# Kernel tuning notes

Measured on AMD Instinct MI355X. Metric: run time of the kernel, lower is better.

The kernel has to match this reference:

```python
import math
import jax, jax.numpy as jnp
from jax import lax
import numpy as np

SR = 48000
N_SAMPLES = 1_440_000
N_TRACKS = 4  # voice, music, ambient, fx

# ---------------- EQ (peaking biquads, Direct Form II transposed) ----------------

def _peak_coefs(freq, gain_db, q):
    A = 10.0 ** (gain_db / 40.0)
    w0 = 2.0 * math.pi * freq / SR
    al = math.sin(w0) / (2.0 * q)
    a0 = 1.0 + al / A
    return ((1.0 + al * A) / a0, -2.0 * math.cos(w0) / a0, (1.0 - al * A) / a0,
            -2.0 * math.cos(w0) / a0, (1.0 - al / A) / a0)

_IDENT = (1.0, 0.0, 0.0, 0.0, 0.0)  # pass-through biquad for padding
_PRESETS = {
    'voice':   [(300.0, -3.0, 0.7), (3000.0, 3.0, 1.0), (8000.0, 2.0, 0.7)],
    'music':   [(80.0, 2.0, 0.7), (5000.0, 1.0, 1.0)],
    'ambient': [(200.0, -2.0, 0.7), (6000.0, -1.0, 0.7)],
    'fx':      [(1000.0, 2.0, 1.0)],
}
_TYPES = ('voice', 'music', 'ambient', 'fx')

def _stage_coefs():
    # [3 stages, 4 tracks, 5 coefs]; missing bands padded with identity biquads
    out = np.zeros((3, N_TRACKS, 5), np.float32)
    for t, ty in enumerate(_TYPES):
        bands = [_peak_coefs(*b) for b in _PRESETS[ty]]
        bands += [_IDENT] * (3 - len(bands))
        for s in range(3):
            out[s, t] = bands[s]
    return out

STAGE_COEFS = _stage_coefs()

def _biquad(x, c):
    # x: [T, C, N], c: [T, 5] -> batched DF2T biquad across tracks/channels
    b0, b1, b2, a1, a2 = (c[:, i][:, None] for i in range(5))
    def step(carry, x_n):  # x_n: [T, C]
        z1, z2 = carry
        y = b0 * x_n + z1
        return (b1 * x_n - a1 * y + z2, b2 * x_n - a2 * y), y
    z = jnp.zeros_like(x[..., 0])
    _, ys = lax.scan(step, (z, z), jnp.moveaxis(x, -1, 0))
    return jnp.moveaxis(ys, 0, -1)

# ---------------- Compressor (envelope follower) ----------------
ATK = math.exp(-1.0 / (10.0 * 0.001 * SR))
REL = math.exp(-1.0 / (100.0 * 0.001 * SR))
THR = 10.0 ** (-18.0 / 20.0)
GR_EXP = 1.0 / 4.0 - 1.0  # ratio = 4

def _compress(x):
    def step(env, x_n):
        lvl = jnp.abs(x_n)
        c = jnp.where(lvl > env, ATK, REL)
        env = c * env + (1.0 - c) * lvl
        gr = jnp.maximum(env / (THR + 1e-8), 1.0) ** GR_EXP
        return env, x_n * gr
    _, ys = lax.scan(step, jnp.zeros_like(x[..., 0]), jnp.moveaxis(x, -1, 0))
    return jnp.moveaxis(ys, 0, -1)

# ---------------- Reverb (Schroeder-Moorer: 4 comb + 2 allpass) ----------------
_BASE = int(SR * 0.03)
COMB_DELAYS = [_BASE, int(_BASE * 1.13), int(_BASE * 1.27), int(_BASE * 1.41)]
AP_DELAYS = [int(SR * 0.005), int(SR * 0.0017)]
FB = 0.3 + 0.5 * 0.6  # room_size = 0.6
WET = 0.3

def _comb(x, delay, fb):
    # y[n] = x[n] + fb*y[n-delay]: `delay` independent 1st-order recurrences
    T, C, N = x.shape
    M = -(-N // delay)
    xp = jnp.pad(x, ((0, 0), (0, 0), (0, M * delay - N))).reshape(T, C, M, delay)
    def step(carry, xm):  # carry/xm: [T, C, delay]
        y = xm + fb * carry
        return y, y
    _, ys = lax.scan(step, jnp.zeros_like(xp[:, :, 0]), jnp.moveaxis(xp, 2, 0))
    return jnp.moveaxis(ys, 0, 2).reshape(T, C, M * delay)[:, :, :N]

def _allpass(x, delay, fb):
    # y[n] = -fb*x[n] + x[n-delay] + fb*y[n-delay] for n>=delay, y[0:delay]=0
    T, C, N = x.shape
    M = -(-N // delay)
    xp = jnp.pad(x, ((0, 0), (0, 0), (0, M * delay - N))).reshape(T, C, M, delay)
    xs = jnp.moveaxis(xp, 2, 0)  # [M, T, C, delay]
    y0 = jnp.zeros_like(xs[0])
    def step(carry, xm):
        x_prev, y_prev = carry
        y = -fb * xm + x_prev + fb * y_prev
        return (xm, y), y
    _, ys = lax.scan(step, (xs[0], y0), xs[1:])
    ys = jnp.concatenate([y0[None], ys], axis=0)
    return jnp.moveaxis(ys, 0, 2).reshape(T, C, M * delay)[:, :, :N]

def _reverb(x):
    wet = sum(_comb(x, d, FB) for d in COMB_DELAYS) / float(len(COMB_DELAYS))
    for d in AP_DELAYS:
        wet = _allpass(wet, d, FB)
    return (1.0 - WET) * x + WET * wet

# ---------------- Full mixer ----------------
CEIL = 10.0 ** (-1.0 / 20.0)  # limiter ceiling, -1 dB

def _forward(tracks, volumes, pans):
    x = tracks  # [4, 2, N]
    for s in range(3):
        x = _biquad(x, jnp.asarray(STAGE_COEFS[s]))
    x = _compress(x)
    # reverb only for ambient (idx 2) and fx (idx 3)
    x = jnp.concatenate([x[:2], _reverb(x[2:])], axis=0)
    angle = (pans + 1.0) * 0.25 * math.pi
    lg = jnp.cos(angle)
    rg = jnp.sin(angle)
    out_l = jnp.einsum('t,tn->n', volumes * lg, x[:, 0])
    out_r = jnp.einsum('t,tn->n', volumes * rg, x[:, 1])
    out = jnp.stack([out_l, out_r])
    return jnp.clip(out, -CEIL, CEIL)


def setup_inputs() -> dict:
    key = jax.random.key(0)
    k1, k2, k3 = jax.random.split(key, 3)
    tracks = jax.random.normal(k1, (N_TRACKS, 2, N_SAMPLES), dtype=jnp.float32)
    volumes = jax.random.uniform(k2, (N_TRACKS,), dtype=jnp.float32)
    pans = jax.random.uniform(k3, (N_TRACKS,), dtype=jnp.float32)
    return {'tracks': tracks, 'volumes': volumes, 'pans': pans}


def reference(tracks, volumes, pans):
    return _forward(tracks, volumes, pans)
```

## Files before the change

### kernel.cpp

```cpp
#include <hip/hip_runtime.h>
#include <math.h>

#define NS  1440000
#define LC  240
#define NCC 6000
#define CHB 94
#define CPW 47
#define EQW 6
#define CWIN (64 + CPW - 1)
#define EWIN (64 + EQW - 1)
#define WPC 121
#define U   24

#define CB  64
#define RVW 40
#define FBC 0.6f

struct Coefs { float c[3][4][5]; };
struct CompC { float atk, rel, rho, invt2; };

__global__ __launch_bounds__(256) void transpose_in(const float* __restrict__ x,
                                                    float* __restrict__ XT) {
  __shared__ float t[16][17];
  int b = blockIdx.x;
  int ch = b / (15 * 375);
  int r  = b % (15 * 375);
  int it = r / 375, jt = r % 375;
  int tx = threadIdx.x & 15, ty = threadIdx.x >> 4;
  int s0 = it * 16, c0 = jt * 16;
  t[ty][tx] = x[(size_t)ch * NS + (size_t)(c0 + ty) * LC + (s0 + tx)];
  __syncthreads();
  XT[(size_t)ch * NS + (size_t)(s0 + ty) * NCC + (c0 + tx)] = t[tx][ty];
}

__device__ inline unsigned int f32_to_bf16_rtne(float v) {
  unsigned int b = __float_as_uint(v);
  return (b + 0x7fffu + ((b >> 16) & 1u)) >> 16;
}

#define EQ_STEPT(VV)                                                       \
  {                                                                        \
    float v = (VV);                                                        \
    _Pragma("unroll")                                                      \
    for (int st = 0; st < NST; ++st) {                                     \
      float ya = fmaf(c[st][0], v, z[st][0]);                              \
      z[st][0] = fmaf(c[st][1], v, z[st][1]) - c[st][3] * ya;              \
      z[st][1] = fmaf(c[st][2], v, -(c[st][4] * ya));                      \
      v = ya;                                                              \
    }                                                                      \
    vout = v;                                                              \
  }

#define EQ_W40T(B)                                                         \
  _Pragma("unroll")                                                        \
  for (int u = 0; u < 20; ++u) {                                           \
    unsigned int wv = (B)[u];                                              \
    float lo = __uint_as_float(wv << 16);                                  \
    float hi = __uint_as_float(wv & 0xffff0000u);                          \
    EQ_STEPT(lo);                                                          \
    EQ_STEPT(hi);                                                          \
  }

template<int NST>
__device__ __forceinline__ void eq_body(const float* __restrict__ X,
                                        float* __restrict__ E,
                                        const Coefs& cf, int tr,
                                        const unsigned int* __restrict__ lds,
                                        int lane, int C0) {
  float c[NST][5];
  #pragma unroll
  for (int st = 0; st < NST; ++st)
    #pragma unroll
    for (int q = 0; q < 5; ++q) c[st][q] = cf.c[st][tr][q];
  float z[NST][2];
  #pragma unroll
  for (int st = 0; st < NST; ++st) { z[st][0] = 0.f; z[st][1] = 0.f; }
  float vout;
  {
    unsigned int b0[20], b1[20];
    const unsigned int* pc = lds + lane * WPC;
    #pragma unroll
    for (int u = 0; u < 20; ++u) b0[u] = pc[u];
    for (int t = 0; t < EQW; ++t) {
      #pragma unroll
      for (int u = 0; u < 20; ++u) b1[u] = pc[20 + u];
      EQ_W40T(b0)
      #pragma unroll
      for (int u = 0; u < 20; ++u) b0[u] = pc[40 + u];
      EQ_W40T(b1)
      #pragma unroll
      for (int u = 0; u < 20; ++u) b1[u] = pc[60 + u];
      EQ_W40T(b0)
      #pragma unroll
      for (int u = 0; u < 20; ++u) b0[u] = pc[80 + u];
      EQ_W40T(b1)
      #pragma unroll
      for (int u = 0; u < 20; ++u) b1[u] = pc[100 + u];
      EQ_W40T(b0)
      pc += WPC;
      #pragma unroll
      for (int u = 0; u < 20; ++u) b0[u] = pc[u];
      EQ_W40T(b1)
    }
  }
  (void)vout;
  int cg = C0 + lane;
  if (cg < NCC) {
    const float* p = X + cg;
    float* q = E + cg;
    float b0[U], b1[U];
    #pragma unroll
    for (int u = 0; u < U; ++u) b0[u] = p[(size_t)u * NCC];
    p += (size_t)U * NCC;
    for (int k = 0; k < 4; ++k) {
      #pragma unroll
      for (int u = 0; u < U; ++u) b1[u] = p[(size_t)u * NCC];
      p += (size_t)U * NCC;
      #pragma unroll
      for (int u = 0; u < U; ++u) { EQ_STEPT(b0[u]); q[(size_t)u * NCC] = vout; }
      q += (size_t)U * NCC;
      #pragma unroll
      for (int u = 0; u < U; ++u) b0[u] = p[(size_t)u * NCC];
      p += (size_t)U * NCC;
      #pragma unroll
      for (int u = 0; u < U; ++u) { EQ_STEPT(b1[u]); q[(size_t)u * NCC] = vout; }
      q += (size_t)U * NCC;
    }
    #pragma unroll
    for (int u = 0; u < U; ++u) b1[u] = p[(size_t)u * NCC];
    #pragma unroll
    for (int u = 0; u < U; ++u) { EQ_STEPT(b0[u]); q[(size_t)u * NCC] = vout; }
    q += (size_t)U * NCC;
    #pragma unroll
    for (int u = 0; u < U; ++u) { EQ_STEPT(b1[u]); q[(size_t)u * NCC] = vout; }
  }
}

__global__ __launch_bounds__(64) void eq_kernel(const float* __restrict__ XT,
                                                float* __restrict__ ET, Coefs cf) {
  __shared__ unsigned int lds[(EWIN + 1) * WPC];
  int blk = blockIdx.x;
  int ch = blk / CHB, cb = blk % CHB;
  int C0 = cb * 64;
  int lane = threadIdx.x;
  int tr = ch >> 1;
  const float* X = XT + (size_t)ch * NS;
  float* E = ET + (size_t)ch * NS;
  const int TOT = EWIN * LC;
  for (int base = 0; base < TOT; base += 256) {
    float v[4]; int sE[4], crE[4]; bool val[4];
    #pragma unroll
    for (int i = 0; i < 4; ++i) {
      int e = base + i * 64 + lane;
      val[i] = e < TOT;
      int ec = val[i] ? e : 0;
      sE[i] = ec / EWIN; crE[i] = ec - sE[i] * EWIN;
      int cg = C0 - EQW + crE[i];
      v[i] = (val[i] && cg >= 0 && cg < NCC) ? X[(size_t)sE[i] * NCC + cg] : 0.f;
    }
    #pragma unroll
    for (int i = 0; i < 4; ++i)
      if (val[i])
        ((unsigned short*)lds)[crE[i] * (2 * WPC) + sE[i]] =
            (unsigned short)f32_to_bf16_rtne(v[i]);
  }
  __syncthreads();
  if (tr == 0)      eq_body<3>(X, E, cf, tr, lds, lane, C0);
  else if (tr == 3) eq_body<1>(X, E, cf, tr, lds, lane, C0);
  else              eq_body<2>(X, E, cf, tr, lds, lane, C0);
}

#define CP_W40(B)                                                          \
  _Pragma("unroll")                                                        \
  for (int u = 0; u < 20; ++u) {                                           \
    unsigned int wv = (B)[u];                                              \
    float lo = __uint_as_float(wv << 16);                                  \
    float hi = __uint_as_float(wv & 0xffff0000u);                          \
    E = fmaxf(fmaf(cc.atk, E, lo), fmaf(cc.rel, E, cc.rho * lo));          \
    E = fmaxf(fmaf(cc.atk, E, hi), fmaf(cc.rel, E, cc.rho * hi));          \
  }

__global__ __launch_bounds__(64) void comp_kernel(const float* __restrict__ ET,
                                                  float* __restrict__ Y, CompC cc) {
  __shared__ unsigned int lds[(CWIN + 1) * WPC];
  int blk = blockIdx.x;
  int ch = blk / CHB, cb = blk % CHB;
  int C0 = cb * 64;
  int lane = threadIdx.x;
  const float* E_ = ET + (size_t)ch * NS;
  const int TOTC = CWIN * LC;
  for (int base = 0; base < TOTC; base += 256) {
    float v[4]; int sE[4], crE[4]; bool val[4];
    #pragma unroll
    for (int i = 0; i < 4; ++i) {
      int e = base + i * 64 + lane;
      val[i] = e < TOTC;
      int ec = val[i] ? e : 0;
      sE[i] = ec / CWIN; crE[i] = ec - sE[i] * CWIN;
      int cg = C0 - CPW + crE[i];
      v[i] = (val[i] && cg >= 0 && cg < NCC) ? E_[(size_t)sE[i] * NCC + cg] : 0.f;
    }
    #pragma unroll
    for (int i = 0; i < 4; ++i)
      if (val[i]) {
        unsigned int b = __float_as_uint(v[i]) & 0x7fffffffu;
        b = (b + 0x7fffu + ((b >> 16) & 1u)) >> 16;
        ((unsigned short*)lds)[crE[i] * (2 * WPC) + sE[i]] = (unsigned short)b;
      }
  }
  __syncthreads();
  float E = 0.f;
  {
    unsigned int b0[20], b1[20];
    const unsigned int* pc = lds + lane * WPC;
    #pragma unroll
    for (int u = 0; u < 20; ++u) b0[u] = pc[u];
    for (int t = 0; t < CPW; ++t) {
      #pragma unroll
      for (int u = 0; u < 20; ++u) b1[u] = pc[20 + u];
      CP_W40(b0)
      #pragma unroll
      for (int u = 0; u < 20; ++u) b0[u] = pc[40 + u];
      CP_W40(b1)
      #pragma unroll
      for (int u = 0; u < 20; ++u) b1[u] = pc[60 + u];
      CP_W40(b0)
      #pragma unroll
      for (int u = 0; u < 20; ++u) b0[u] = pc[80 + u];
      CP_W40(b1)
      #pragma unroll
      for (int u = 0; u < 20; ++u) b1[u] = pc[100 + u];
      CP_W40(b0)
      pc += WPC;
      #pragma unroll
      for (int u = 0; u < 20; ++u) b0[u] = pc[u];
      CP_W40(b1)
    }
  }
  int cg = C0 + lane;
  if (cg < NCC) {
    const float* p = E_ + cg;
    float* py = Y + (size_t)ch * NS + (size_t)cg * LC;
    float b0[U], b1[U];
    #pragma unroll
    for (int u = 0; u < U; ++u) b0[u] = p[(size_t)u * NCC];
    p += (size_t)U * NCC;
    #define CP_OUT(BUF)                                                       \
      _Pragma("unroll")                                                       \
      for (int u = 0; u < U; ++u) {                                           \
        float v = BUF[u];                                                     \
        float lvl = fabsf(v);                                                 \
        E = fmaxf(fmaf(cc.atk, E, lvl), fmaf(cc.rel, E, cc.rho * lvl));       \
        float m = fmaxf(E * cc.invt2, 1.0f);                                  \
        py[u] = v * (sqrtf(sqrtf(m)) * __builtin_amdgcn_rcpf(m));             \
      }                                                                       \
      py += U;
    for (int k = 0; k < 4; ++k) {
      #pragma unroll
      for (int u = 0; u < U; ++u) b1[u] = p[(size_t)u * NCC];
      p += (size_t)U * NCC;
      CP_OUT(b0)
      #pragma unroll
      for (int u = 0; u < U; ++u) b0[u] = p[(size_t)u * NCC];
      p += (size_t)U * NCC;
      CP_OUT(b1)
    }
    #pragma unroll
    for (int u = 0; u < U; ++u) b1[u] = p[(size_t)u * NCC];
    CP_OUT(b0)
    CP_OUT(b1)
  }
}

__global__ __launch_bounds__(256) void comb_kernel(const float* __restrict__ xin,
                                                   float* __restrict__ acc,
                                                   int d, int J, int first) {
  int tid = blockIdx.x * 256 + threadIdx.x;
  int total = 4 * d * J;
  if (tid >= total) return;
  int rch = tid / (d * J);
  int rem = tid - rch * (d * J);
  int j = rem / d;
  int p = rem - j * d;
  const float* xi = xin + (size_t)(4 + rch) * NS;
  float* ao = acc + (size_t)rch * NS;
  int K = (NS - p + d - 1) / d;
  int kstart = j * CB;
  if (kstart >= K) return;
  int kend = kstart + CB; if (kend > K) kend = K;
  float yv = 0.f;
  int k = (j == 0) ? 0 : (kstart - RVW);
  int n = k * d + p;
  if (j != 0) {
    #pragma unroll 16
    for (; k < kstart; ++k, n += d) yv = fmaf(FBC, yv, xi[n]);
  }
  if (first) {
    #pragma unroll 16
    for (; k < kend; ++k, n += d) { yv = fmaf(FBC, yv, xi[n]); ao[n] = yv; }
  } else {
    #pragma unroll 16
    for (; k < kend; ++k, n += d) { yv = fmaf(FBC, yv, xi[n]); ao[n] += yv; }
  }
}

__global__ __launch_bounds__(256) void allpass_kernel(const float* __restrict__ xin,
                                                      float* __restrict__ yout,
                                                      int d, int J, float inscale) {
  int tid = blockIdx.x * 256 + threadIdx.x;
  int total = 4 * d * J;
  if (tid >= total) return;
  int rch = tid / (d * J);
  int rem = tid - rch * (d * J);
  int j = rem / d;
  int p = rem - j * d;
  const float* xi = xin + (size_t)rch * NS;
  float* yo = yout + (size_t)rch * NS;
  int K = (NS - p + d - 1) / d;
  int kstart = j * CB;
  if (kstart >= K) return;
  int kend = kstart + CB; if (kend > K) kend = K;
  float yv = 0.f;
  int k;
  if (j == 0) { yo[p] = 0.f; k = 1; }
  else        { k = kstart - RVW; }
  int n = k * d + p;
  if (j != 0) {
    #pragma unroll 16
    for (; k < kstart; ++k, n += d) {
      float u  = inscale * xi[n];
      float up = inscale * xi[n - d];
      yv = fmaf(FBC, yv, fmaf(-FBC, u, up));
    }
  }
  #pragma unroll 16
  for (; k < kend; ++k, n += d) {
    float u  = inscale * xi[n];
    float up = inscale * xi[n - d];
    yv = fmaf(FBC, yv, fmaf(-FBC, u, up));
    yo[n] = yv;
  }
}

__global__ __launch_bounds__(256) void mix_kernel(const float* __restrict__ cp,
                                                  const float* __restrict__ wet,
                                                  const float* __restrict__ vol,
                                                  const float* __restrict__ pan,
                                                  float* __restrict__ out) {
  int i = blockIdx.x * 256 + threadIdx.x;
  if (i >= NS / 4) return;
  size_t n = (size_t)i * 4;
  float g[8];
  #pragma unroll
  for (int t = 0; t < 4; ++t) {
    float angle = (pan[t] + 1.0f) * 0.25f * 3.14159265358979323846f;
    g[2 * t]     = vol[t] * cosf(angle);
    g[2 * t + 1] = vol[t] * sinf(angle);
  }
  const float CEIL = 0.89125093813374556f;
  float4 t0l = *(const float4*)(cp + 0 * (size_t)NS + n);
  float4 t0r = *(const float4*)(cp + 1 * (size_t)NS + n);
  float4 t1l = *(const float4*)(cp + 2 * (size_t)NS + n);
  float4 t1r = *(const float4*)(cp + 3 * (size_t)NS + n);
  float4 t2l = *(const float4*)(cp + 4 * (size_t)NS + n);
  float4 t2r = *(const float4*)(cp + 5 * (size_t)NS + n);
  float4 t3l = *(const float4*)(cp + 6 * (size_t)NS + n);
  float4 t3r = *(const float4*)(cp + 7 * (size_t)NS + n);
  float4 w2l = *(const float4*)(wet + 0 * (size_t)NS + n);
  float4 w2r = *(const float4*)(wet + 1 * (size_t)NS + n);
  float4 w3l = *(const float4*)(wet + 2 * (size_t)NS + n);
  float4 w3r = *(const float4*)(wet + 3 * (size_t)NS + n);
  float4 outl, outr;
  float* pl = &outl.x; float* pr = &outr.x;
  const float* a0 = &t0l.x; const float* a1 = &t0r.x;
  const float* a2 = &t1l.x; const float* a3 = &t1r.x;
  const float* a4 = &t2l.x; const float* a5 = &t2r.x;
  const float* a6 = &t3l.x; const float* a7 = &t3r.x;
  const float* b4 = &w2l.x; const float* b5 = &w2r.x;
  const float* b6 = &w3l.x; const float* b7 = &w3r.x;
  #pragma unroll
  for (int cc = 0; cc < 4; ++cc) {
    float x4 = 0.7f * a4[cc] + 0.3f * b4[cc];
    float x5 = 0.7f * a5[cc] + 0.3f * b5[cc];
    float x6 = 0.7f * a6[cc] + 0.3f * b6[cc];
    float x7 = 0.7f * a7[cc] + 0.3f * b7[cc];
    float Lv = g[0] * a0[cc] + g[2] * a2[cc] + g[4] * x4 + g[6] * x6;
    float Rv = g[1] * a1[cc] + g[3] * a3[cc] + g[5] * x5 + g[7] * x7;
    pl[cc] = fminf(fmaxf(Lv, -CEIL), CEIL);
    pr[cc] = fminf(fmaxf(Rv, -CEIL), CEIL);
  }
  *(float4*)(out + n) = outl;
  *(float4*)(out + (size_t)NS + n) = outr;
}

static void peak_coefs(double f, double gdb, double q, float* o) {
  double A  = pow(10.0, gdb / 40.0);
  double w0 = 2.0 * M_PI * f / 48000.0;
  double al = sin(w0) / (2.0 * q);
  double a0 = 1.0 + al / A;
  o[0] = (float)((1.0 + al * A) / a0);
  o[1] = (float)(-2.0 * cos(w0) / a0);
  o[2] = (float)((1.0 - al * A) / a0);
  o[3] = (float)(-2.0 * cos(w0) / a0);
  o[4] = (float)((1.0 - al / A) / a0);
}

extern "C" void kernel_launch(void* const* d_in, const int* in_sizes, int n_in,
                              void* d_out, int out_size, void* d_ws, size_t ws_size,
                              hipStream_t stream) {
  const float* tracks = (const float*)d_in[0];
  const float* vols   = (const float*)d_in[1];
  const float* pans   = (const float*)d_in[2];
  float* out = (float*)d_out;
  float* w = (float*)d_ws;
  float* XT    = w;
  float* ET    = w + (size_t)8 * NS;
  float* cpbuf = w;
  float* combb = w + (size_t)8 * NS;
  float* apb   = w + (size_t)12 * NS;
  float* wet2  = w + (size_t)8 * NS;

  Coefs cf;
  const float ident[5] = {1.f, 0.f, 0.f, 0.f, 0.f};
  const double P[4][3][3] = {
    {{300, -3, 0.7}, {3000, 3, 1.0}, {8000, 2, 0.7}},
    {{80, 2, 0.7},   {5000, 1, 1.0}, {0, 0, 0}},
    {{200, -2, 0.7}, {6000, -1, 0.7}, {0, 0, 0}},
    {{1000, 2, 1.0}, {0, 0, 0},      {0, 0, 0}},
  };
  const int nb[4] = {3, 2, 2, 1};
  for (int t = 0; t < 4; ++t)
    for (int s = 0; s < 3; ++s) {
      if (s < nb[t]) peak_coefs(P[t][s][0], P[t][s][1], P[t][s][2], cf.c[s][t]);
      else for (int q = 0; q < 5; ++q) cf.c[s][t][q] = ident[q];
    }

  CompC cc;
  double atk = exp(-1.0 / 480.0), rel = exp(-1.0 / 4800.0);
  double oatk = 1.0 - atk, orel = 1.0 - rel;
  double invt = 1.0 / (pow(10.0, -18.0 / 20.0) + 1e-8);
  cc.atk   = (float)atk;
  cc.rel   = (float)rel;
  cc.rho   = (float)(orel / oatk);
  cc.invt2 = (float)(oatk * invt);

  hipLaunchKernelGGL(transpose_in, dim3(8 * 15 * 375), dim3(256), 0, stream,
                     tracks, XT);
  hipLaunchKernelGGL(eq_kernel, dim3(8 * CHB), dim3(64), 0, stream,
                     XT, ET, cf);
  hipLaunchKernelGGL(comp_kernel, dim3(8 * CHB), dim3(64), 0, stream,
                     ET, cpbuf, cc);

  const int combd[4] = {1440, 1627, 1828, 2030};
  for (int i = 0; i < 4; ++i) {
    int d = combd[i];
    int K = (NS + d - 1) / d;
    int J = (K + CB - 1) / CB;
    int total = 4 * d * J;
    hipLaunchKernelGGL(comb_kernel, dim3((total + 255) / 256), dim3(256), 0, stream,
                       cpbuf, combb, d, J, (i == 0) ? 1 : 0);
  }
  {
    int d = 240, K = (NS + d - 1) / d, J = (K + CB - 1) / CB, total = 4 * d * J;
    hipLaunchKernelGGL(allpass_kernel, dim3((total + 255) / 256), dim3(256), 0, stream,
                       combb, apb, d, J, 0.25f);
  }
  {
    int d = 81, K = (NS + d - 1) / d, J = (K + CB - 1) / CB, total = 4 * d * J;
    hipLaunchKernelGGL(allpass_kernel, dim3((total + 255) / 256), dim3(256), 0, stream,
                       apb, wet2, d, J, 1.0f);
  }
  hipLaunchKernelGGL(mix_kernel, dim3((NS / 4 + 255) / 256), dim3(256), 0, stream,
                     cpbuf, wet2, vols, pans, out);
}
```

Before: 534.5 us.

## Drop input transpose, enlarge compressor blocks, fuse comb filters with atomics

Removes the transpose_in kernel, so the EQ and compressor kernels read the original sample-major layout directly, with each lane walking its own contiguous chunk. The compressor uses 256-thread blocks with a larger dynamic-LDS window, which cuts the redundant warm-up overlap per block, and it packs the attack/release envelope update into 2-wide vector math. The four comb-filter launches become one launch that accumulates into a zeroed buffer with atomic adds. The trade-offs are strided uncoalesced per-lane reads in place of coalesced ones, atomic traffic in place of plain stores, and an extra memset.

```diff
diff --git a/kernel.cpp b/kernel.cpp
--- a/kernel.cpp
+++ b/kernel.cpp
@@ -7,8 +7,9 @@
 #define CHB 94
 #define CPW 47
 #define EQW 6
-#define CWIN (64 + CPW - 1)
 #define EWIN (64 + EQW - 1)
+#define CPB 256
+#define CWIN2 (CPB + CPW - 1)
 #define WPC 121
 #define U   24
 
@@ -16,22 +17,10 @@
 #define RVW 40
 #define FBC 0.6f
 
+typedef float v2f __attribute__((ext_vector_type(2)));
+
 struct Coefs { float c[3][4][5]; };
 struct CompC { float atk, rel, rho, invt2; };
-
-__global__ __launch_bounds__(256) void transpose_in(const float* __restrict__ x,
-                                                    float* __restrict__ XT) {
-  __shared__ float t[16][17];
-  int b = blockIdx.x;
-  int ch = b / (15 * 375);
-  int r  = b % (15 * 375);
-  int it = r / 375, jt = r % 375;
-  int tx = threadIdx.x & 15, ty = threadIdx.x >> 4;
-  int s0 = it * 16, c0 = jt * 16;
-  t[ty][tx] = x[(size_t)ch * NS + (size_t)(c0 + ty) * LC + (s0 + tx)];
-  __syncthreads();
-  XT[(size_t)ch * NS + (size_t)(s0 + ty) * NCC + (c0 + tx)] = t[tx][ty];
-}
 
 __device__ inline unsigned int f32_to_bf16_rtne(float v) {
   unsigned int b = __float_as_uint(v);
@@ -106,37 +95,37 @@
   (void)vout;
   int cg = C0 + lane;
   if (cg < NCC) {
-    const float* p = X + cg;
-    float* q = E + cg;
+    const float* p = X + (size_t)cg * LC;
+    float* q = E + (size_t)cg * LC;
     float b0[U], b1[U];
     #pragma unroll
-    for (int u = 0; u < U; ++u) b0[u] = p[(size_t)u * NCC];
-    p += (size_t)U * NCC;
+    for (int u = 0; u < U; ++u) b0[u] = p[u];
+    p += U;
     for (int k = 0; k < 4; ++k) {
       #pragma unroll
-      for (int u = 0; u < U; ++u) b1[u] = p[(size_t)u * NCC];
-      p += (size_t)U * NCC;
-      #pragma unroll
-      for (int u = 0; u < U; ++u) { EQ_STEPT(b0[u]); q[(size_t)u * NCC] = vout; }
-      q += (size_t)U * NCC;
-      #pragma unroll
-      for (int u = 0; u < U; ++u) b0[u] = p[(size_t)u * NCC];
-      p += (size_t)U * NCC;
-      #pragma unroll
-      for (int u = 0; u < U; ++u) { EQ_STEPT(b1[u]); q[(size_t)u * NCC] = vout; }
-      q += (size_t)U * NCC;
-    }
-    #pragma unroll
-    for (int u = 0; u < U; ++u) b1[u] = p[(size_t)u * NCC];
-    #pragma unroll
-    for (int u = 0; u < U; ++u) { EQ_STEPT(b0[u]); q[(size_t)u * NCC] = vout; }
-    q += (size_t)U * NCC;
-    #pragma unroll
-    for (int u = 0; u < U; ++u) { EQ_STEPT(b1[u]); q[(size_t)u * NCC] = vout; }
-  }
-}
-
-__global__ __launch_bounds__(64) void eq_kernel(const float* __restrict__ XT,
+      for (int u = 0; u < U; ++u) b1[u] = p[u];
+      p += U;
+      #pragma unroll
+      for (int u = 0; u < U; ++u) { EQ_STEPT(b0[u]); q[u] = vout; }
+      q += U;
+      #pragma unroll
+      for (int u = 0; u < U; ++u) b0[u] = p[u];
+      p += U;
+      #pragma unroll
+      for (int u = 0; u < U; ++u) { EQ_STEPT(b1[u]); q[u] = vout; }
+      q += U;
+    }
+    #pragma unroll
+    for (int u = 0; u < U; ++u) b1[u] = p[u];
+    #pragma unroll
+    for (int u = 0; u < U; ++u) { EQ_STEPT(b0[u]); q[u] = vout; }
+    q += U;
+    #pragma unroll
+    for (int u = 0; u < U; ++u) { EQ_STEPT(b1[u]); q[u] = vout; }
+  }
+}
+
+__global__ __launch_bounds__(64) void eq_kernel(const float* __restrict__ X0,
                                                 float* __restrict__ ET, Coefs cf) {
   __shared__ unsigned int lds[(EWIN + 1) * WPC];
   int blk = blockIdx.x;
@@ -144,24 +133,24 @@
   int C0 = cb * 64;
   int lane = threadIdx.x;
   int tr = ch >> 1;
-  const float* X = XT + (size_t)ch * NS;
+  const float* X = X0 + (size_t)ch * NS;
   float* E = ET + (size_t)ch * NS;
   const int TOT = EWIN * LC;
   for (int base = 0; base < TOT; base += 256) {
-    float v[4]; int sE[4], crE[4]; bool val[4];
+    float v[4]; int colE[4], sE[4]; bool val[4];
     #pragma unroll
     for (int i = 0; i < 4; ++i) {
       int e = base + i * 64 + lane;
       val[i] = e < TOT;
       int ec = val[i] ? e : 0;
-      sE[i] = ec / EWIN; crE[i] = ec - sE[i] * EWIN;
-      int cg = C0 - EQW + crE[i];
-      v[i] = (val[i] && cg >= 0 && cg < NCC) ? X[(size_t)sE[i] * NCC + cg] : 0.f;
+      colE[i] = ec / LC; sE[i] = ec - colE[i] * LC;
+      int cg = C0 - EQW + colE[i];
+      v[i] = (val[i] && cg >= 0 && cg < NCC) ? X[(size_t)cg * LC + sE[i]] : 0.f;
     }
     #pragma unroll
     for (int i = 0; i < 4; ++i)
       if (val[i])
-        ((unsigned short*)lds)[crE[i] * (2 * WPC) + sE[i]] =
+        ((unsigned short*)lds)[colE[i] * (2 * WPC) + sE[i]] =
             (unsigned short)f32_to_bf16_rtne(v[i]);
   }
   __syncthreads();
@@ -169,6 +158,11 @@
   else if (tr == 3) eq_body<1>(X, E, cf, tr, lds, lane, C0);
   else              eq_body<2>(X, E, cf, tr, lds, lane, C0);
 }
+
+#define CP_STEP1(VX)                                                       \
+  { v2f t = OQ * (v2f){(VX), (VX)};                                        \
+    v2f e2 = AR * (v2f){E, E} + t;                                         \
+    E = fmaxf(e2.x, e2.y); }
 
 #define CP_W40(B)                                                          \
   _Pragma("unroll")                                                        \
@@ -176,43 +170,45 @@
     unsigned int wv = (B)[u];                                              \
     float lo = __uint_as_float(wv << 16);                                  \
     float hi = __uint_as_float(wv & 0xffff0000u);                          \
-    E = fmaxf(fmaf(cc.atk, E, lo), fmaf(cc.rel, E, cc.rho * lo));          \
-    E = fmaxf(fmaf(cc.atk, E, hi), fmaf(cc.rel, E, cc.rho * hi));          \
-  }
-
-__global__ __launch_bounds__(64) void comp_kernel(const float* __restrict__ ET,
-                                                  float* __restrict__ Y, CompC cc) {
-  __shared__ unsigned int lds[(CWIN + 1) * WPC];
+    CP_STEP1(lo);                                                          \
+    CP_STEP1(hi);                                                          \
+  }
+
+__global__ __launch_bounds__(256) void comp_kernel(const float* __restrict__ ET,
+                                                   float* __restrict__ Y, CompC cc) {
+  extern __shared__ unsigned int lds[];
   int blk = blockIdx.x;
-  int ch = blk / CHB, cb = blk % CHB;
-  int C0 = cb * 64;
-  int lane = threadIdx.x;
+  int ch = blk / 24, cb = blk % 24;
+  int C0 = cb * CPB;
+  int tid = threadIdx.x;
   const float* E_ = ET + (size_t)ch * NS;
-  const int TOTC = CWIN * LC;
-  for (int base = 0; base < TOTC; base += 256) {
-    float v[4]; int sE[4], crE[4]; bool val[4];
+  const v2f AR = {cc.atk, cc.rel};
+  const v2f OQ = {1.0f, cc.rho};
+  const int TOT2 = CWIN2 * LC;
+  for (int base = 0; base < TOT2; base += 1024) {
+    float v[4]; int colE[4], sE[4]; bool val[4];
     #pragma unroll
     for (int i = 0; i < 4; ++i) {
-      int e = base + i * 64 + lane;
-      val[i] = e < TOTC;
+      int e = base + i * 256 + tid;
+      val[i] = e < TOT2;
       int ec = val[i] ? e : 0;
-      sE[i] = ec / CWIN; crE[i] = ec - sE[i] * CWIN;
-      int cg = C0 - CPW + crE[i];
-      v[i] = (val[i] && cg >= 0 && cg < NCC) ? E_[(size_t)sE[i] * NCC + cg] : 0.f;
+      colE[i] = ec / LC; sE[i] = ec - colE[i] * LC;
+      int cg = C0 - CPW + colE[i];
+      v[i] = (val[i] && cg >= 0 && cg < NCC) ? E_[(size_t)cg * LC + sE[i]] : 0.f;
     }
     #pragma unroll
     for (int i = 0; i < 4; ++i)
       if (val[i]) {
         unsigned int b = __float_as_uint(v[i]) & 0x7fffffffu;
         b = (b + 0x7fffu + ((b >> 16) & 1u)) >> 16;
-        ((unsigned short*)lds)[crE[i] * (2 * WPC) + sE[i]] = (unsigned short)b;
+        ((unsigned short*)lds)[colE[i] * (2 * WPC) + sE[i]] = (unsigned short)b;
       }
   }
   __syncthreads();
   float E = 0.f;
   {
     unsigned int b0[20], b1[20];
-    const unsigned int* pc = lds + lane * WPC;
+    const unsigned int* pc = lds + tid * WPC;
     #pragma unroll
     for (int u = 0; u < 20; ++u) b0[u] = pc[u];
     for (int t = 0; t < CPW; ++t) {
@@ -237,14 +233,14 @@
       CP_W40(b1)
     }
   }
-  int cg = C0 + lane;
+  int cg = C0 + tid;
   if (cg < NCC) {
-    const float* p = E_ + cg;
+    const float* p = E_ + (size_t)cg * LC;
     float* py = Y + (size_t)ch * NS + (size_t)cg * LC;
     float b0[U], b1[U];
     #pragma unroll
-    for (int u = 0; u < U; ++u) b0[u] = p[(size_t)u * NCC];
-    p += (size_t)U * NCC;
+    for (int u = 0; u < U; ++u) b0[u] = p[u];
+    p += U;
     #define CP_OUT(BUF)                                                       \
       _Pragma("unroll")                                                       \
       for (int u = 0; u < U; ++u) {                                           \
@@ -257,29 +253,33 @@
       py += U;
     for (int k = 0; k < 4; ++k) {
       #pragma unroll
-      for (int u = 0; u < U; ++u) b1[u] = p[(size_t)u * NCC];
-      p += (size_t)U * NCC;
+      for (int u = 0; u < U; ++u) b1[u] = p[u];
+      p += U;
       CP_OUT(b0)
       #pragma unroll
-      for (int u = 0; u < U; ++u) b0[u] = p[(size_t)u * NCC];
-      p += (size_t)U * NCC;
+      for (int u = 0; u < U; ++u) b0[u] = p[u];
+      p += U;
       CP_OUT(b1)
     }
     #pragma unroll
-    for (int u = 0; u < U; ++u) b1[u] = p[(size_t)u * NCC];
+    for (int u = 0; u < U; ++u) b1[u] = p[u];
     CP_OUT(b0)
     CP_OUT(b1)
   }
 }
 
-__global__ __launch_bounds__(256) void comb_kernel(const float* __restrict__ xin,
-                                                   float* __restrict__ acc,
-                                                   int d, int J, int first) {
+__global__ __launch_bounds__(256) void comb_fused(const float* __restrict__ xin,
+                                                  float* __restrict__ acc,
+                                                  int4 dv, int4 Jv, int4 bv, int total) {
   int tid = blockIdx.x * 256 + threadIdx.x;
-  int total = 4 * d * J;
   if (tid >= total) return;
-  int rch = tid / (d * J);
-  int rem = tid - rch * (d * J);
+  int d, J, rel;
+  if      (tid < bv.y) { d = dv.x; J = Jv.x; rel = tid; }
+  else if (tid < bv.z) { d = dv.y; J = Jv.y; rel = tid - bv.y; }
+  else if (tid < bv.w) { d = dv.z; J = Jv.z; rel = tid - bv.z; }
+  else                 { d = dv.w; J = Jv.w; rel = tid - bv.w; }
+  int rch = rel / (d * J);
+  int rem = rel - rch * (d * J);
   int j = rem / d;
   int p = rem - j * d;
   const float* xi = xin + (size_t)(4 + rch) * NS;
@@ -295,12 +295,10 @@
     #pragma unroll 16
     for (; k < kstart; ++k, n += d) yv = fmaf(FBC, yv, xi[n]);
   }
-  if (first) {
-    #pragma unroll 16
-    for (; k < kend; ++k, n += d) { yv = fmaf(FBC, yv, xi[n]); ao[n] = yv; }
-  } else {
-    #pragma unroll 16
-    for (; k < kend; ++k, n += d) { yv = fmaf(FBC, yv, xi[n]); ao[n] += yv; }
+  #pragma unroll 16
+  for (; k < kend; ++k, n += d) {
+    yv = fmaf(FBC, yv, xi[n]);
+    unsafeAtomicAdd(&ao[n], yv);
   }
 }
 
@@ -413,7 +411,6 @@
   const float* pans   = (const float*)d_in[2];
   float* out = (float*)d_out;
   float* w = (float*)d_ws;
-  float* XT    = w;
   float* ET    = w + (size_t)8 * NS;
   float* cpbuf = w;
   float* combb = w + (size_t)8 * NS;
@@ -444,21 +441,30 @@
   cc.rho   = (float)(orel / oatk);
   cc.invt2 = (float)(oatk * invt);
 
-  hipLaunchKernelGGL(transpose_in, dim3(8 * 15 * 375), dim3(256), 0, stream,
-                     tracks, XT);
   hipLaunchKernelGGL(eq_kernel, dim3(8 * CHB), dim3(64), 0, stream,
-                     XT, ET, cf);
-  hipLaunchKernelGGL(comp_kernel, dim3(8 * CHB), dim3(64), 0, stream,
+                     tracks, ET, cf);
+
+  const int compLDS = (CWIN2 + 1) * WPC * 4;
+  hipFuncSetAttribute((const void*)comp_kernel,
+                      hipFuncAttributeMaxDynamicSharedMemorySize, compLDS);
+  hipLaunchKernelGGL(comp_kernel, dim3(8 * 24), dim3(256), compLDS, stream,
                      ET, cpbuf, cc);
 
-  const int combd[4] = {1440, 1627, 1828, 2030};
-  for (int i = 0; i < 4; ++i) {
-    int d = combd[i];
-    int K = (NS + d - 1) / d;
-    int J = (K + CB - 1) / CB;
-    int total = 4 * d * J;
-    hipLaunchKernelGGL(comb_kernel, dim3((total + 255) / 256), dim3(256), 0, stream,
-                       cpbuf, combb, d, J, (i == 0) ? 1 : 0);
+  hipMemsetAsync(combb, 0, (size_t)4 * NS * sizeof(float), stream);
+  {
+    const int ds[4] = {1440, 1627, 1828, 2030};
+    int Js[4], base[4], tot = 0;
+    for (int i = 0; i < 4; ++i) {
+      int K = (NS + ds[i] - 1) / ds[i];
+      Js[i] = (K + CB - 1) / CB;
+      base[i] = tot;
+      tot += 4 * ds[i] * Js[i];
+    }
+    int4 dv = {ds[0], ds[1], ds[2], ds[3]};
+    int4 Jv = {Js[0], Js[1], Js[2], Js[3]};
+    int4 bv = {base[0], base[1], base[2], base[3]};
+    hipLaunchKernelGGL(comb_fused, dim3((tot + 255) / 256), dim3(256), 0, stream,
+                       cpbuf, combb, dv, Jv, bv, tot);
   }
   {
     int d = 240, K = (NS + d - 1) / d, J = (K + CB - 1) / CB, total = 4 * d * J;
```

Measured after the change: 483.8 us. 1.1x faster.
